# Performance work log

Measured on AMD Instinct MI355X. Metric: run time of the kernel, lower is better.

The kernel has to match this reference:

```python
import jax, jax.numpy as jnp
import numpy as np

DIM = 192
HEADS = 6
HEAD_DIM = 32
WS = 7          # window_size
DISP = WS // 2  # cyclic-shift displacement = 3
NEG = -1e9      # large negative instead of -inf (grad-safe, numerically equivalent)


def _rel_indices():
    idx = np.array([[x, y] for x in range(WS) for y in range(WS)])  # [WS^2, 2]
    d = idx[None, :, :] - idx[:, None, :] + WS - 1                  # [WS^2, WS^2, 2]
    return d


def _shift_masks():
    n = WS * WS
    ul = np.zeros((n, n), dtype=np.float32)
    ul[-DISP * WS:, :-DISP * WS] = NEG
    ul[:-DISP * WS, -DISP * WS:] = NEG
    lr = np.zeros((WS, WS, WS, WS), dtype=np.float32)
    lr[:, -DISP:, :, :-DISP] = NEG
    lr[:, :-DISP, :, -DISP:] = NEG
    lr = lr.reshape(n, n)
    return ul, lr


def setup_inputs() -> dict:
    key = jax.random.key(0)
    k1, k2, k3, k4, k5 = jax.random.split(key, 5)
    inner = HEADS * HEAD_DIM
    B, H, W = 32, 56, 56
    x = jax.random.normal(k1, (B, H, W, DIM), dtype=jnp.float32)
    w_qkv = jax.random.normal(k2, (DIM, inner * 3), dtype=jnp.float32) * (DIM ** -0.5)
    w_out = jax.random.normal(k3, (inner, DIM), dtype=jnp.float32) * (inner ** -0.5)
    b_out = jnp.zeros((DIM,), dtype=jnp.float32)
    pos_emb = jax.random.normal(k4, (2 * WS - 1, 2 * WS - 1), dtype=jnp.float32)
    return {"x": x, "w_qkv": w_qkv, "w_out": w_out, "b_out": b_out, "pos_emb": pos_emb}


def _forward(x, w_qkv, w_out, b_out, pos_emb):
    b, n_h, n_w, _ = x.shape
    nw_h, nw_w = n_h // WS, n_w // WS
    nw = nw_h * nw_w
    n = WS * WS
    scale = HEAD_DIM ** -0.5

    # cyclic shift
    x = jnp.roll(x, shift=(-DISP, -DISP), axis=(1, 2))

    qkv = x @ w_qkv  # [b, H, W, 3*inner]
    qkv = qkv.reshape(b, nw_h, WS, nw_w, WS, 3, HEADS, HEAD_DIM)
    # -> [3, b, heads, nw, WS*WS, head_dim]
    qkv = qkv.transpose(5, 0, 6, 1, 3, 2, 4, 7).reshape(3, b, HEADS, nw, n, HEAD_DIM)
    q, k, v = qkv[0], qkv[1], qkv[2]

    dots = jnp.einsum('bhwid,bhwjd->bhwij', q, k) * scale  # [b,h,nw,n,n]

    rel = _rel_indices()
    bias = pos_emb[rel[:, :, 0], rel[:, :, 1]]  # [n, n]
    dots = dots + bias

    # shifted-window masks: last row of windows gets UL mask, last column gets LR mask
    ul, lr = _shift_masks()
    madd = jnp.zeros((nw, n, n), dtype=dots.dtype)
    madd = madd.at[-nw_w:].add(jnp.asarray(ul))
    madd = madd.at[nw_w - 1::nw_w].add(jnp.asarray(lr))
    dots = dots + madd

    attn = jax.nn.softmax(dots, axis=-1)
    out = jnp.einsum('bhwij,bhwjd->bhwid', attn, v)  # [b,h,nw,n,hd]

    # un-window: -> [b, H, W, inner]
    out = out.reshape(b, HEADS, nw_h, nw_w, WS, WS, HEAD_DIM)
    out = out.transpose(0, 2, 4, 3, 5, 1, 6).reshape(b, n_h, n_w, HEADS * HEAD_DIM)
    out = out @ w_out + b_out

    # cyclic back-shift
    out = jnp.roll(out, shift=(DISP, DISP), axis=(1, 2))
    return out


def reference(x, w_qkv, w_out, b_out, pos_emb):
    return _forward(x, w_qkv, w_out, b_out, pos_emb)
```

## Files before the change

### kernel.cpp

```cpp
#include <hip/hip_runtime.h>
#include <hip/hip_bf16.h>


typedef __bf16 bf16x8 __attribute__((ext_vector_type(8)));
typedef __bf16 bf16x4 __attribute__((ext_vector_type(4)));
typedef float f32x4 __attribute__((ext_vector_type(4)));
using bf = __bf16;

#define MFMA16(a, b, c) __builtin_amdgcn_mfma_f32_16x16x32_bf16((a), (b), (c), 0, 0, 0)

static constexpr float kNEG = -1000000000.0f;
static constexpr float kScale = 0.17677669529663687f;

static constexpr size_t OFF_WQKVT = 0;
static constexpr size_t OFF_WOUTT = 221184;
static constexpr size_t OFF_TBL   = 294912;

static constexpr int QK_STRIDE = 40;
static constexpr int VT_STRIDE = 72;
static constexpr int X_STRIDE  = 200;
static constexpr int O_STRIDE  = 200;
static constexpr int TB_STRIDE = 68;
static constexpr int R0_OFF = 0;
static constexpr int R1_OFF = 23552;
static constexpr int R2_OFF = 47104;
static constexpr int TB_OFF = 74752;
static constexpr int LDS_BYTES = TB_OFF + 49 * TB_STRIDE * 2 + 8;

__device__ __forceinline__ unsigned pack2(float a, float b) {
  union { bf h[2]; unsigned u; } cv;
  cv.h[0] = (bf)a; cv.h[1] = (bf)b;
  return cv.u;
}

__global__ void prep_kernel(const float* __restrict__ wqkv, const float* __restrict__ wout,
                            const float* __restrict__ pos, char* __restrict__ ws) {
  bf* wqkvT = (bf*)(ws + OFF_WQKVT);
  bf* woutT = (bf*)(ws + OFF_WOUTT);
  float* tbl = (float*)(ws + OFF_TBL);
  int tid = blockIdx.x * blockDim.x + threadIdx.x;
  int nthr = gridDim.x * blockDim.x;
  for (int i = tid; i < 192 * 576; i += nthr) {
    int k = i / 576, n = i % 576;
    wqkvT[n * 192 + k] = (bf)wqkv[i];
  }
  for (int i = tid; i < 192 * 192; i += nthr) {
    int k = i / 192, n = i % 192;
    woutT[n * 192 + k] = (bf)wout[i];
  }
  for (int i = tid; i < 4 * 64 * 64; i += nthr) {
    int type = i >> 12, rem = i & 4095, r = rem >> 6, c = rem & 63;
    float v;
    if (r < 49 && c < 49) {
      int ix = r / 7, iy = r % 7, jx = c / 7, jy = c % 7;
      v = pos[(jx - ix + 6) * 13 + (jy - iy + 6)];
      if ((type & 1) && ((r >= 28) != (c >= 28))) v += kNEG;
      if ((type & 2) && ((iy >= 4) != (jy >= 4))) v += kNEG;
    } else {
      v = kNEG;
    }
    tbl[i] = v;
  }
}

__global__ __launch_bounds__(512, 4) void fused_kernel(const float* __restrict__ x,
                                                       const float* __restrict__ bout,
                                                       const char* __restrict__ ws,
                                                       float* __restrict__ out) {
  __shared__ __align__(16) char smem[LDS_BYTES];
  bf* Xl = (bf*)(smem + R0_OFF);
  bf* Ql = (bf*)(smem + R0_OFF);
  bf* Kl = (bf*)(smem + R1_OFF);
  bf* Ol = (bf*)(smem + R1_OFF);
  bf* Vl = (bf*)(smem + R2_OFF);
  bf* Tb = (bf*)(smem + TB_OFF);

  const bf* wqkvT = (const bf*)(ws + OFF_WQKVT);
  const bf* woutT = (const bf*)(ws + OFF_WOUTT);

  int bw = blockIdx.x;
  int b = bw >> 6, win = bw & 63;
  int wh = win >> 3, wwi = win & 7;
  int type = ((wh == 7) ? 1 : 0) | ((wwi == 7) ? 2 : 0);
  const float* tblg = (const float*)(ws + OFF_TBL) + type * 4096;

  int tid = threadIdx.x;
  int wave = tid >> 6, lane = tid & 63;
  int l15 = lane & 15, g = lane >> 4;
  int mrow = wave >> 2, ncol = wave & 3;

#pragma unroll
  for (int it = 0; it < 3; ++it) {
    int chunk = it * 512 + tid;
    if (chunk < 1176) {
      int r = chunk / 24, c8 = (chunk % 24) * 8;
      int tr = r / 7, tc = r % 7;
      int h = wh * 7 + tr + 3; if (h >= 56) h -= 56;
      int w = wwi * 7 + tc + 3; if (w >= 56) w -= 56;
      const float* p = x + (((size_t)b * 56 + h) * 56 + w) * 192 + c8;
      bf16x8 v;
#pragma unroll
      for (int j = 0; j < 8; ++j) v[j] = (bf)p[j];
      *(bf16x8*)(Xl + r * X_STRIDE + c8) = v;
    }
  }
  if (tid < 392) {
    int r = tid >> 3, c8 = (tid & 7) * 8;
    const float* p = tblg + r * 64 + c8;
    bf16x4 v0, v1;
#pragma unroll
    for (int j = 0; j < 4; ++j) { v0[j] = (bf)p[j]; v1[j] = (bf)p[4 + j]; }
    *(bf16x4*)(Tb + r * TB_STRIDE + c8) = v0;
    *(bf16x4*)(Tb + r * TB_STRIDE + c8 + 4) = v1;
  }
  __syncthreads();

  {
    f32x4 acc[2][6] = {};
#pragma unroll
    for (int ks = 0; ks < 6; ++ks) {
      bf16x8 a[2];
#pragma unroll
      for (int mt = 0; mt < 2; ++mt) {
        int t = mrow * 32 + mt * 16 + l15; if (t > 48) t = 48;
        a[mt] = *(const bf16x8*)(Xl + t * X_STRIDE + ks * 32 + g * 8);
      }
#pragma unroll
      for (int nt = 0; nt < 6; ++nt) {
        int n = 192 + ncol * 96 + nt * 16 + l15;
        bf16x8 bfr = *(const bf16x8*)(wqkvT + (size_t)n * 192 + ks * 32 + g * 8);
#pragma unroll
        for (int mt = 0; mt < 2; ++mt) acc[mt][nt] = MFMA16(a[mt], bfr, acc[mt][nt]);
      }
    }
#pragma unroll
    for (int nt = 0; nt < 6; ++nt) {
      int n = 192 + ncol * 96 + nt * 16 + l15;
      int s3 = n / 192;
      int lc = n - s3 * 192;
      int hd = lc >> 5, d = lc & 31;
#pragma unroll
      for (int mt = 0; mt < 2; ++mt) {
#pragma unroll
        for (int r = 0; r < 4; ++r) {
          int t = mrow * 32 + mt * 16 + 4 * g + r;
          bf bv = (bf)acc[mt][nt][r];
          if (s3 == 1) { if (t < 49) Kl[(hd * 49 + t) * QK_STRIDE + d] = bv; }
          else         { Vl[(hd * 32 + d) * VT_STRIDE + t] = bv; }
        }
      }
    }
  }

  {
    f32x4 qacc[2][3] = {};
#pragma unroll
    for (int ks = 0; ks < 6; ++ks) {
      bf16x8 a[2];
#pragma unroll
      for (int mt = 0; mt < 2; ++mt) {
        int t = mrow * 32 + mt * 16 + l15; if (t > 48) t = 48;
        a[mt] = *(const bf16x8*)(Xl + t * X_STRIDE + ks * 32 + g * 8);
      }
#pragma unroll
      for (int nt = 0; nt < 3; ++nt) {
        int n = ncol * 48 + nt * 16 + l15;
        bf16x8 bfr = *(const bf16x8*)(wqkvT + (size_t)n * 192 + ks * 32 + g * 8);
#pragma unroll
        for (int mt = 0; mt < 2; ++mt) qacc[mt][nt] = MFMA16(a[mt], bfr, qacc[mt][nt]);
      }
    }
    __syncthreads();
#pragma unroll
    for (int nt = 0; nt < 3; ++nt) {
      int n = ncol * 48 + nt * 16 + l15;
      int hd = n >> 5, d = n & 31;
#pragma unroll
      for (int mt = 0; mt < 2; ++mt) {
#pragma unroll
        for (int r = 0; r < 4; ++r) {
          int t = mrow * 32 + mt * 16 + 4 * g + r;
          if (t < 49) Ql[(hd * 49 + t) * QK_STRIDE + d] = (bf)qacc[mt][nt][r];
        }
      }
    }
  }
  __syncthreads();

  unsigned pp[3][4][2];
#pragma unroll
  for (int ii = 0; ii < 3; ++ii) {
    int item = wave + ii * 8;
    int head = item >> 2, mq = item & 3;
    const bf* Qh = Ql + head * 49 * QK_STRIDE;
    const bf* Kh = Kl + head * 49 * QK_STRIDE;

    int q = mq * 16 + l15;
    int qc = q > 48 ? 48 : q;
    bf16x8 qf = *(const bf16x8*)(Qh + qc * QK_STRIDE + g * 8);

    f32x4 sa[4];
#pragma unroll
    for (int T = 0; T < 4; ++T) {
      int kt = ((l15 >> 2) << 3) + ((T & 1) << 2) + ((T >> 1) << 5) + (l15 & 3);
      int ktc = kt > 48 ? 48 : kt;
      bf16x8 kf = *(const bf16x8*)(Kh + ktc * QK_STRIDE + g * 8);
      f32x4 z = {};
      sa[T] = MFMA16(kf, qf, z);
    }

    float e[4][4];
    float lsum = 0.0f;
#pragma unroll
    for (int T = 0; T < 4; ++T) {
      int cb = (g << 3) + ((T & 1) << 2) + ((T >> 1) << 5);
      bf16x4 bias = *(const bf16x4*)(Tb + qc * TB_STRIDE + cb);
#pragma unroll
      for (int r = 0; r < 4; ++r) {
        float ev = __expf(sa[T][r] * kScale + (float)bias[r]);
        e[T][r] = ev;
        lsum += ev;
      }
    }
    lsum += __shfl_xor(lsum, 16);
    lsum += __shfl_xor(lsum, 32);
    float rinv = 1.0f / lsum;
#pragma unroll
    for (int T = 0; T < 4; ++T) {
      pp[ii][T][0] = pack2(e[T][0] * rinv, e[T][1] * rinv);
      pp[ii][T][1] = pack2(e[T][2] * rinv, e[T][3] * rinv);
    }
  }
  __syncthreads();

  for (int ii = 0; ii < 3; ++ii) {
    int item = wave + ii * 8;
    int head = item >> 2, mq = item & 3;
    const bf* Vh = Vl + head * 32 * VT_STRIDE;

    f32x4 o0 = {}, o1 = {};
#pragma unroll
    for (int ks = 0; ks < 2; ++ks) {
      union { unsigned u[4]; bf16x8 v; } af;
      af.u[0] = pp[ii][2 * ks][0];
      af.u[1] = pp[ii][2 * ks][1];
      af.u[2] = pp[ii][2 * ks + 1][0];
      af.u[3] = pp[ii][2 * ks + 1][1];
      bf16x8 v0 = *(const bf16x8*)(Vh + l15 * VT_STRIDE + ks * 32 + g * 8);
      bf16x8 v1 = *(const bf16x8*)(Vh + (16 + l15) * VT_STRIDE + ks * 32 + g * 8);
      o0 = MFMA16(af.v, v0, o0);
      o1 = MFMA16(af.v, v1, o1);
    }
#pragma unroll
    for (int r = 0; r < 4; ++r) {
      int orow = mq * 16 + 4 * g + r;
      if (orow < 49) {
        Ol[orow * O_STRIDE + head * 32 + l15]      = (bf)o0[r];
        Ol[orow * O_STRIDE + head * 32 + 16 + l15] = (bf)o1[r];
      }
    }
  }
  __syncthreads();

  f32x4 pacc[2][3] = {};
#pragma unroll
  for (int ks = 0; ks < 6; ++ks) {
    int t0 = mrow * 32 + l15;      if (t0 > 48) t0 = 48;
    int t1 = mrow * 32 + 16 + l15; if (t1 > 48) t1 = 48;
    bf16x8 a0 = *(const bf16x8*)(Ol + t0 * O_STRIDE + ks * 32 + g * 8);
    bf16x8 a1 = *(const bf16x8*)(Ol + t1 * O_STRIDE + ks * 32 + g * 8);
#pragma unroll
    for (int nt = 0; nt < 3; ++nt) {
      bf16x8 bfr = *(const bf16x8*)(woutT + (size_t)(ncol * 48 + nt * 16 + l15) * 192 + ks * 32 + g * 8);
      pacc[0][nt] = MFMA16(a0, bfr, pacc[0][nt]);
      pacc[1][nt] = MFMA16(a1, bfr, pacc[1][nt]);
    }
  }
#pragma unroll
  for (int nt = 0; nt < 3; ++nt) {
    int col = ncol * 48 + nt * 16 + l15;
    float bo = bout[col];
#pragma unroll
    for (int mt = 0; mt < 2; ++mt) {
#pragma unroll
      for (int r = 0; r < 4; ++r) {
        int t = mrow * 32 + mt * 16 + 4 * g + r;
        if (t < 49) {
          int tr = t / 7, tc = t % 7;
          int h = wh * 7 + tr + 3; if (h >= 56) h -= 56;
          int w2 = wwi * 7 + tc + 3; if (w2 >= 56) w2 -= 56;
          out[(((size_t)b * 56 + h) * 56 + w2) * 192 + col] = pacc[mt][nt][r] + bo;
        }
      }
    }
  }
}

extern "C" void kernel_launch(void* const* d_in, const int* in_sizes, int n_in,
                              void* d_out, int out_size, void* d_ws, size_t ws_size,
                              hipStream_t stream) {
  const float* x = (const float*)d_in[0];
  const float* wqkv = (const float*)d_in[1];
  const float* wout = (const float*)d_in[2];
  const float* bout = (const float*)d_in[3];
  const float* pos = (const float*)d_in[4];
  char* ws = (char*)d_ws;

  hipLaunchKernelGGL(prep_kernel, dim3(128), dim3(256), 0, stream, wqkv, wout, pos, ws);
  hipLaunchKernelGGL(fused_kernel, dim3(2048), dim3(512), 0, stream,
                     x, bout, (const char*)ws, (float*)d_out);
}
```

Baseline: 172.9 us.

## Split fused window-attention kernel into QKV, attention and projection kernels

The single fused per-window kernel is replaced by three kernels: a QKV projection kernel that writes Q, K and transposed V to global workspace, a per-(window,head) attention kernel with small blocks, and an output-projection kernel that reads the attention output back. The aim is to cut LDS usage and raise occupancy and parallelism in each stage. In exchange it adds roughly 150 MB of extra global memory traffic for the intermediates, plus two extra launches.

```diff
diff --git a/kernel.cpp b/kernel.cpp
--- a/kernel.cpp
+++ b/kernel.cpp
@@ -14,18 +14,15 @@
 
 static constexpr size_t OFF_WQKVT = 0;
 static constexpr size_t OFF_WOUTT = 221184;
-static constexpr size_t OFF_TBL   = 294912;
-
-static constexpr int QK_STRIDE = 40;
-static constexpr int VT_STRIDE = 72;
-static constexpr int X_STRIDE  = 200;
-static constexpr int O_STRIDE  = 200;
-static constexpr int TB_STRIDE = 68;
-static constexpr int R0_OFF = 0;
-static constexpr int R1_OFF = 23552;
-static constexpr int R2_OFF = 47104;
-static constexpr int TB_OFF = 74752;
-static constexpr int LDS_BYTES = TB_OFF + 49 * TB_STRIDE * 2 + 8;
+static constexpr size_t OFF_TBLBF = 294912;
+static constexpr size_t OFF_QG    = 321568;
+static constexpr size_t OFF_KG    = OFF_QG + 38535168ull;
+static constexpr size_t OFF_VT    = OFF_KG + 38535168ull;
+static constexpr size_t OFF_O2    = OFF_VT + 50331648ull;
+
+static constexpr int VT_STR   = 64;
+static constexpr int X_STRIDE = 200;
+static constexpr int O_STRIDE = 200;
 
 __device__ __forceinline__ unsigned pack2(float a, float b) {
   union { bf h[2]; unsigned u; } cv;
@@ -37,7 +34,7 @@
                             const float* __restrict__ pos, char* __restrict__ ws) {
   bf* wqkvT = (bf*)(ws + OFF_WQKVT);
   bf* woutT = (bf*)(ws + OFF_WOUTT);
-  float* tbl = (float*)(ws + OFF_TBL);
+  bf* tblbf = (bf*)(ws + OFF_TBLBF);
   int tid = blockIdx.x * blockDim.x + threadIdx.x;
   int nthr = gridDim.x * blockDim.x;
   for (int i = tid; i < 192 * 576; i += nthr) {
@@ -48,41 +45,35 @@
     int k = i / 192, n = i % 192;
     woutT[n * 192 + k] = (bf)wout[i];
   }
-  for (int i = tid; i < 4 * 64 * 64; i += nthr) {
-    int type = i >> 12, rem = i & 4095, r = rem >> 6, c = rem & 63;
-    float v;
-    if (r < 49 && c < 49) {
-      int ix = r / 7, iy = r % 7, jx = c / 7, jy = c % 7;
-      v = pos[(jx - ix + 6) * 13 + (jy - iy + 6)];
-      if ((type & 1) && ((r >= 28) != (c >= 28))) v += kNEG;
-      if ((type & 2) && ((iy >= 4) != (jy >= 4))) v += kNEG;
-    } else {
-      v = kNEG;
-    }
-    tbl[i] = v;
-  }
-}
-
-__global__ __launch_bounds__(512, 4) void fused_kernel(const float* __restrict__ x,
-                                                       const float* __restrict__ bout,
-                                                       const char* __restrict__ ws,
-                                                       float* __restrict__ out) {
-  __shared__ __align__(16) char smem[LDS_BYTES];
-  bf* Xl = (bf*)(smem + R0_OFF);
-  bf* Ql = (bf*)(smem + R0_OFF);
-  bf* Kl = (bf*)(smem + R1_OFF);
-  bf* Ol = (bf*)(smem + R1_OFF);
-  bf* Vl = (bf*)(smem + R2_OFF);
-  bf* Tb = (bf*)(smem + TB_OFF);
+  for (int i = tid; i < 4 * 49 * 68; i += nthr) {
+    int type = i / (49 * 68), rem = i % (49 * 68), r = rem / 68, c = rem % 68;
+    float v = 0.0f;
+    if (c < 64) {
+      if (c < 49) {
+        int ix = r / 7, iy = r % 7, jx = c / 7, jy = c % 7;
+        v = pos[(jx - ix + 6) * 13 + (jy - iy + 6)];
+        if ((type & 1) && ((r >= 28) != (c >= 28))) v += kNEG;
+        if ((type & 2) && ((iy >= 4) != (jy >= 4))) v += kNEG;
+      } else {
+        v = kNEG;
+      }
+    }
+    tblbf[i] = (bf)v;
+  }
+}
+
+__global__ __launch_bounds__(512, 6) void qkv_kernel(const float* __restrict__ x,
+                                                     char* __restrict__ ws) {
+  __shared__ __align__(16) bf Xl[49 * X_STRIDE];
 
   const bf* wqkvT = (const bf*)(ws + OFF_WQKVT);
-  const bf* woutT = (const bf*)(ws + OFF_WOUTT);
+  bf* Qg = (bf*)(ws + OFF_QG);
+  bf* Kg = (bf*)(ws + OFF_KG);
+  bf* VT = (bf*)(ws + OFF_VT);
 
   int bw = blockIdx.x;
   int b = bw >> 6, win = bw & 63;
   int wh = win >> 3, wwi = win & 7;
-  int type = ((wh == 7) ? 1 : 0) | ((wwi == 7) ? 2 : 0);
-  const float* tblg = (const float*)(ws + OFF_TBL) + type * 4096;
 
   int tid = threadIdx.x;
   int wave = tid >> 6, lane = tid & 63;
@@ -104,15 +95,6 @@
       *(bf16x8*)(Xl + r * X_STRIDE + c8) = v;
     }
   }
-  if (tid < 392) {
-    int r = tid >> 3, c8 = (tid & 7) * 8;
-    const float* p = tblg + r * 64 + c8;
-    bf16x4 v0, v1;
-#pragma unroll
-    for (int j = 0; j < 4; ++j) { v0[j] = (bf)p[j]; v1[j] = (bf)p[4 + j]; }
-    *(bf16x4*)(Tb + r * TB_STRIDE + c8) = v0;
-    *(bf16x4*)(Tb + r * TB_STRIDE + c8 + 4) = v1;
-  }
   __syncthreads();
 
   {
@@ -137,16 +119,21 @@
     for (int nt = 0; nt < 6; ++nt) {
       int n = 192 + ncol * 96 + nt * 16 + l15;
       int s3 = n / 192;
-      int lc = n - s3 * 192;
-      int hd = lc >> 5, d = lc & 31;
+      int c = n - s3 * 192;
 #pragma unroll
       for (int mt = 0; mt < 2; ++mt) {
-#pragma unroll
-        for (int r = 0; r < 4; ++r) {
-          int t = mrow * 32 + mt * 16 + 4 * g + r;
-          bf bv = (bf)acc[mt][nt][r];
-          if (s3 == 1) { if (t < 49) Kl[(hd * 49 + t) * QK_STRIDE + d] = bv; }
-          else         { Vl[(hd * 32 + d) * VT_STRIDE + t] = bv; }
+        if (s3 == 1) {
+#pragma unroll
+          for (int r = 0; r < 4; ++r) {
+            int t = mrow * 32 + mt * 16 + 4 * g + r;
+            if (t < 49) Kg[((size_t)bw * 49 + t) * 192 + c] = (bf)acc[mt][nt][r];
+          }
+        } else {
+          int tb4 = mrow * 32 + mt * 16 + 4 * g;
+          union { unsigned u[2]; } pk;
+          pk.u[0] = pack2(acc[mt][nt][0], acc[mt][nt][1]);
+          pk.u[1] = pack2(acc[mt][nt][2], acc[mt][nt][3]);
+          *(uint2*)(VT + ((size_t)bw * 192 + c) * VT_STR + tb4) = *(uint2*)pk.u;
         }
       }
     }
@@ -170,41 +157,52 @@
         for (int mt = 0; mt < 2; ++mt) qacc[mt][nt] = MFMA16(a[mt], bfr, qacc[mt][nt]);
       }
     }
-    __syncthreads();
 #pragma unroll
     for (int nt = 0; nt < 3; ++nt) {
       int n = ncol * 48 + nt * 16 + l15;
-      int hd = n >> 5, d = n & 31;
 #pragma unroll
       for (int mt = 0; mt < 2; ++mt) {
 #pragma unroll
         for (int r = 0; r < 4; ++r) {
           int t = mrow * 32 + mt * 16 + 4 * g + r;
-          if (t < 49) Ql[(hd * 49 + t) * QK_STRIDE + d] = (bf)qacc[mt][nt][r];
+          if (t < 49) Qg[((size_t)bw * 49 + t) * 192 + n] = (bf)qacc[mt][nt][r];
         }
       }
     }
   }
-  __syncthreads();
-
-  unsigned pp[3][4][2];
-#pragma unroll
-  for (int ii = 0; ii < 3; ++ii) {
-    int item = wave + ii * 8;
-    int head = item >> 2, mq = item & 3;
-    const bf* Qh = Ql + head * 49 * QK_STRIDE;
-    const bf* Kh = Kl + head * 49 * QK_STRIDE;
-
+}
+
+__global__ __launch_bounds__(128, 6) void attn_kernel(const char* __restrict__ ws) {
+  int id = blockIdx.x;
+  int bw = id / 6, head = id - bw * 6;
+  int win = bw & 63;
+  int wh = win >> 3, wwi = win & 7;
+  int type = ((wh == 7) ? 1 : 0) | ((wwi == 7) ? 2 : 0);
+
+  const bf* Qh = (const bf*)(ws + OFF_QG) + (size_t)bw * 49 * 192 + head * 32;
+  const bf* Kh = (const bf*)(ws + OFF_KG) + (size_t)bw * 49 * 192 + head * 32;
+  const bf* Vh = (const bf*)(ws + OFF_VT) + ((size_t)bw * 192 + head * 32) * VT_STR;
+  const bf* Tb = (const bf*)(ws + OFF_TBLBF) + type * 49 * 68;
+  bf* O2 = (bf*)(ws + OFF_O2) + (size_t)bw * 49 * 192 + head * 32;
+
+  int tid = threadIdx.x;
+  int wave = tid >> 6, lane = tid & 63;
+  int l15 = lane & 15, g = lane >> 4;
+
+  unsigned pp[2][4][2];
+#pragma unroll
+  for (int ii = 0; ii < 2; ++ii) {
+    int mq = wave * 2 + ii;
     int q = mq * 16 + l15;
     int qc = q > 48 ? 48 : q;
-    bf16x8 qf = *(const bf16x8*)(Qh + qc * QK_STRIDE + g * 8);
+    bf16x8 qf = *(const bf16x8*)(Qh + (size_t)qc * 192 + g * 8);
 
     f32x4 sa[4];
 #pragma unroll
     for (int T = 0; T < 4; ++T) {
       int kt = ((l15 >> 2) << 3) + ((T & 1) << 2) + ((T >> 1) << 5) + (l15 & 3);
       int ktc = kt > 48 ? 48 : kt;
-      bf16x8 kf = *(const bf16x8*)(Kh + ktc * QK_STRIDE + g * 8);
+      bf16x8 kf = *(const bf16x8*)(Kh + (size_t)ktc * 192 + g * 8);
       f32x4 z = {};
       sa[T] = MFMA16(kf, qf, z);
     }
@@ -214,7 +212,7 @@
 #pragma unroll
     for (int T = 0; T < 4; ++T) {
       int cb = (g << 3) + ((T & 1) << 2) + ((T >> 1) << 5);
-      bf16x4 bias = *(const bf16x4*)(Tb + qc * TB_STRIDE + cb);
+      bf16x4 bias = *(const bf16x4*)(Tb + qc * 68 + cb);
 #pragma unroll
       for (int r = 0; r < 4; ++r) {
         float ev = __expf(sa[T][r] * kScale + (float)bias[r]);
@@ -231,13 +229,10 @@
       pp[ii][T][1] = pack2(e[T][2] * rinv, e[T][3] * rinv);
     }
   }
-  __syncthreads();
-
-  for (int ii = 0; ii < 3; ++ii) {
-    int item = wave + ii * 8;
-    int head = item >> 2, mq = item & 3;
-    const bf* Vh = Vl + head * 32 * VT_STRIDE;
-
+
+#pragma unroll
+  for (int ii = 0; ii < 2; ++ii) {
+    int mq = wave * 2 + ii;
     f32x4 o0 = {}, o1 = {};
 #pragma unroll
     for (int ks = 0; ks < 2; ++ks) {
@@ -246,8 +241,8 @@
       af.u[1] = pp[ii][2 * ks][1];
       af.u[2] = pp[ii][2 * ks + 1][0];
       af.u[3] = pp[ii][2 * ks + 1][1];
-      bf16x8 v0 = *(const bf16x8*)(Vh + l15 * VT_STRIDE + ks * 32 + g * 8);
-      bf16x8 v1 = *(const bf16x8*)(Vh + (16 + l15) * VT_STRIDE + ks * 32 + g * 8);
+      bf16x8 v0 = *(const bf16x8*)(Vh + (size_t)l15 * VT_STR + ks * 32 + g * 8);
+      bf16x8 v1 = *(const bf16x8*)(Vh + (size_t)(16 + l15) * VT_STR + ks * 32 + g * 8);
       o0 = MFMA16(af.v, v0, o0);
       o1 = MFMA16(af.v, v1, o1);
     }
@@ -255,9 +250,37 @@
     for (int r = 0; r < 4; ++r) {
       int orow = mq * 16 + 4 * g + r;
       if (orow < 49) {
-        Ol[orow * O_STRIDE + head * 32 + l15]      = (bf)o0[r];
-        Ol[orow * O_STRIDE + head * 32 + 16 + l15] = (bf)o1[r];
-      }
+        O2[(size_t)orow * 192 + l15]      = (bf)o0[r];
+        O2[(size_t)orow * 192 + 16 + l15] = (bf)o1[r];
+      }
+    }
+  }
+}
+
+__global__ __launch_bounds__(512, 8) void proj_kernel(const float* __restrict__ bout,
+                                                      const char* __restrict__ ws,
+                                                      float* __restrict__ out) {
+  __shared__ __align__(16) bf Ol[49 * O_STRIDE];
+
+  const bf* woutT = (const bf*)(ws + OFF_WOUTT);
+  const bf* O2 = (const bf*)(ws + OFF_O2);
+
+  int bw = blockIdx.x;
+  int b = bw >> 6, win = bw & 63;
+  int wh = win >> 3, wwi = win & 7;
+
+  int tid = threadIdx.x;
+  int wave = tid >> 6, lane = tid & 63;
+  int l15 = lane & 15, g = lane >> 4;
+  int mrow = wave >> 2, ncol = wave & 3;
+
+#pragma unroll
+  for (int it = 0; it < 3; ++it) {
+    int chunk = it * 512 + tid;
+    if (chunk < 1176) {
+      int r = chunk / 24, c8 = (chunk % 24) * 8;
+      *(bf16x8*)(Ol + r * O_STRIDE + c8) =
+          *(const bf16x8*)(O2 + ((size_t)bw * 49 + r) * 192 + c8);
     }
   }
   __syncthreads();
@@ -307,6 +330,7 @@
   char* ws = (char*)d_ws;
 
   hipLaunchKernelGGL(prep_kernel, dim3(128), dim3(256), 0, stream, wqkv, wout, pos, ws);
-  hipLaunchKernelGGL(fused_kernel, dim3(2048), dim3(512), 0, stream,
-                     x, bout, (const char*)ws, (float*)d_out);
-}
+  hipLaunchKernelGGL(qkv_kernel, dim3(2048), dim3(512), 0, stream, x, ws);
+  hipLaunchKernelGGL(attn_kernel, dim3(12288), dim3(128), 0, stream, (const char*)ws);
+  hipLaunchKernelGGL(proj_kernel, dim3(2048), dim3(512), 0, stream, bout, (const char*)ws, (float*)d_out);
+}
```

Result: slower. 309.2 us (+78.9%).
